# Performance work log

Hardware: AMD Instinct MI355X
Metric: run time of the kernel (lower is better)

The kernel has to match this reference:

```python
import jax, jax.numpy as jnp
import numpy as np

H, D = 8, 128           # num_heads, head_dim
HID = 1024              # hidden_size
K = 4                   # short conv kernel
EPS_QK = 1e-6
EPS_NORM = 1e-5


def short_conv(x, w):
    # x: (B, T, C), w: (C, 1, K) depthwise causal conv (zero initial state) + SiLU
    k = w.shape[-1]
    xp = jnp.pad(x, ((0, 0), (k - 1, 0), (0, 0)))
    xc = jnp.transpose(xp, (0, 2, 1))  # (B, C, T+K-1)
    y = jax.lax.conv_general_dilated(xc, w, window_strides=(1,), padding='VALID',
                                     feature_group_count=w.shape[0])
    return jax.nn.silu(jnp.transpose(y, (0, 2, 1)))


def _rmsn(t, eps):
    return t * jax.lax.rsqrt(jnp.mean(t * t, axis=-1, keepdims=True) + eps)


def setup_inputs() -> dict:
    key = jax.random.key(0)
    ks = jax.random.split(key, 16)
    s = 0.02
    inp = {
        'x': jax.random.normal(ks[0], (2, 1024, HID), dtype=jnp.float32),
        'Wq': jax.random.normal(ks[1], (H * D, HID), dtype=jnp.float32) * s,
        'Wk': jax.random.normal(ks[2], (H * D, HID), dtype=jnp.float32) * s,
        'Wv': jax.random.normal(ks[3], (H * D, HID), dtype=jnp.float32) * s,
        'wq_conv': jax.random.normal(ks[4], (H * D, 1, K), dtype=jnp.float32) * 0.3,
        'wk_conv': jax.random.normal(ks[5], (H * D, 1, K), dtype=jnp.float32) * 0.3,
        'wv_conv': jax.random.normal(ks[6], (H * D, 1, K), dtype=jnp.float32) * 0.3,
        'Wfa': jax.random.normal(ks[7], (D, HID), dtype=jnp.float32) * s,
        'Wfb': jax.random.normal(ks[8], (H * D, D), dtype=jnp.float32) * s,
        'Wb': jax.random.normal(ks[9], (H, HID), dtype=jnp.float32) * s,
        'Wga': jax.random.normal(ks[10], (D, HID), dtype=jnp.float32) * s,
        'Wgb': jax.random.normal(ks[11], (H * D, D), dtype=jnp.float32) * s,
        'A_log': jnp.log(jax.random.uniform(ks[12], (H,), minval=1.0, maxval=16.0, dtype=jnp.float32)),
        'dt_bias': jnp.zeros((H, D), dtype=jnp.float32),
        'o_norm_w': jnp.ones((D,), dtype=jnp.float32),
        'Wo': jax.random.normal(ks[13], (HID, H * D), dtype=jnp.float32) * s,
    }
    return inp


def reference(x, Wq, Wk, Wv, wq_conv, wk_conv, wv_conv, Wfa, Wfb, Wb, Wga, Wgb,
              A_log, dt_bias, o_norm_w, Wo):
    B, T, _ = x.shape
    scale = float(D) ** -0.5

    q = short_conv(x @ Wq.T, wq_conv).reshape(B, T, H, D)
    k = short_conv(x @ Wk.T, wk_conv).reshape(B, T, H, D)
    v = short_conv(x @ Wv.T, wv_conv).reshape(B, T, H, D)

    q = (scale ** 2) * _rmsn(q, EPS_QK)
    k = scale * _rmsn(k, EPS_QK)

    a_logits = ((x @ Wfa.T) @ Wfb.T).reshape(B, T, H, D)
    g = -jnp.exp(A_log)[None, None, :, None] * jax.nn.softplus(a_logits + dt_bias)  # (B,T,H,D)
    beta = jax.nn.sigmoid(x @ Wb.T)  # (B,T,H)

    # gated delta-rule recurrence over time; state S: (B, H, Dk, Dv)
    def step(S, inputs):
        q_t, k_t, v_t, g_t, b_t = inputs
        S = S * jnp.exp(g_t)[..., None]                       # per-channel decay on key dim
        kv = jnp.einsum('bhd,bhdv->bhv', k_t, S)              # read
        delta = b_t[..., None] * (v_t - kv)                   # beta-gated delta
        S = S + k_t[..., None] * delta[:, :, None, :]         # rank-1 write
        o = jnp.einsum('bhd,bhdv->bhv', q_t, S)
        return S, o

    tb = lambda t: jnp.moveaxis(t, 1, 0)  # (B,T,...) -> (T,B,...)
    S0 = jnp.zeros((B, H, D, D), dtype=x.dtype)
    _, o_t = jax.lax.scan(step, S0, (tb(q), tb(k), tb(v), tb(g), tb(beta)))
    out = jnp.moveaxis(o_t, 0, 1)  # (B, T, H, D)

    gate = ((x @ Wga.T) @ Wgb.T).reshape(B, T, H, D)
    out = _rmsn(out, EPS_NORM) * o_norm_w * jax.nn.sigmoid(gate)
    return out.reshape(B, T, H * D) @ Wo.T
```

## Files before the change

### kernel.cpp

```cpp
#include <hip/hip_runtime.h>
#include <hip/hip_bf16.h>
#include <math.h>

#define H 8
#define D 128
#define HID 1024
#define KCONV 4
#define G 8

typedef __bf16 bhalf;
typedef __bf16 bhalf4 __attribute__((ext_vector_type(4)));
typedef __bf16 bhalf8 __attribute__((ext_vector_type(8)));
typedef float f32x4 __attribute__((ext_vector_type(4)));
typedef float f32x2 __attribute__((ext_vector_type(2)));

__device__ __forceinline__ void async16(const void* g, void* l) {
    __builtin_amdgcn_global_load_lds(
        (const __attribute__((address_space(1))) void*)g,
        (__attribute__((address_space(3))) void*)l, 16, 0, 0);
}
__device__ __forceinline__ void async4(const void* g, void* l) {
    __builtin_amdgcn_global_load_lds(
        (const __attribute__((address_space(1))) void*)g,
        (__attribute__((address_space(3))) void*)l, 4, 0, 0);
}

__device__ __forceinline__ f32x4 ds2_b64(const float* p) {
    f32x4 r;
    asm volatile("ds_read2_b64 %0, %1 offset0:0 offset1:64"
                 : "=v"(r)
                 : "v"((const __attribute__((address_space(3))) float*)p));
    return r;
}
__device__ __forceinline__ f32x2 ds2_b32_o128(const float* p) {
    f32x2 r;
    asm volatile("ds_read2_b32 %0, %1 offset0:0 offset1:128"
                 : "=v"(r)
                 : "v"((const __attribute__((address_space(3))) float*)p));
    return r;
}
__device__ __forceinline__ f32x2 ds2_b32_o1(const float* p) {
    f32x2 r;
    asm volatile("ds_read2_b32 %0, %1 offset0:0 offset1:1"
                 : "=v"(r)
                 : "v"((const __attribute__((address_space(3))) float*)p));
    return r;
}

__global__ __launch_bounds__(256) void gemm_bf16_nt(const bhalf* A, const bhalf* B,
                                                    void* Cv,
                                                    int M, int N, int K,
                                                    int lda, int ldb, int ldc, int epi,
                                                    const float* __restrict__ A_log,
                                                    const float* __restrict__ dt_bias,
                                                    const bhalf* A2, const bhalf* B2,
                                                    void* C2, int epi2,
                                                    bhalf* __restrict__ pXAG,
                                                    float* __restrict__ pBETA)
{
    if (blockIdx.z) { A = A2; B = B2; Cv = C2; epi = epi2; }
    __shared__ __align__(16) bhalf As[128][32];
    __shared__ __align__(16) bhalf Bs[64][32];
    int tid = threadIdx.x;
    int wid = tid >> 6, lane = tid & 63;
    int rowBase = blockIdx.y * 128;
    int colBase = blockIdx.x * 64;
    int wm = wid >> 1, wn = wid & 1;

    f32x4 acc[4][2] = {};

    int r = lane >> 2;
    int cseg = lane & 3;

    for (int k0 = 0; k0 < K; k0 += 32) {
        __syncthreads();
#pragma unroll
        for (int s = 0; s < 3; ++s) {
            int j = wid * 3 + s;
            if (j < 8) {
                const bhalf* ga = A + (size_t)(rowBase + j * 16 + r) * lda + k0 + cseg * 8;
                async16(ga, &As[j * 16][0]);
            } else {
                int jb = j - 8;
                const bhalf* ga = B + (size_t)(colBase + jb * 16 + r) * ldb + k0 + cseg * 8;
                async16(ga, &Bs[jb * 16][0]);
            }
        }
        __syncthreads();
        int mq = lane & 15, kq = (lane >> 4) * 8;
        bhalf8 af[4], bfr[2];
#pragma unroll
        for (int mt = 0; mt < 4; ++mt)
            af[mt] = *(const bhalf8*)&As[wm * 64 + mt * 16 + mq][kq];
#pragma unroll
        for (int nt = 0; nt < 2; ++nt)
            bfr[nt] = *(const bhalf8*)&Bs[wn * 32 + nt * 16 + mq][kq];
#pragma unroll
        for (int mt = 0; mt < 4; ++mt)
#pragma unroll
            for (int nt = 0; nt < 2; ++nt)
                acc[mt][nt] = __builtin_amdgcn_mfma_f32_16x16x32_bf16(
                    af[mt], bfr[nt], acc[mt][nt], 0, 0, 0);
    }
    int rquad = (lane >> 4) * 4;
#pragma unroll
    for (int mt = 0; mt < 4; ++mt) {
        int m0 = rowBase + wm * 64 + mt * 16 + rquad;
#pragma unroll
        for (int nt = 0; nt < 2; ++nt) {
            int c = colBase + wn * 32 + (lane & 15) + nt * 16;
#pragma unroll
            for (int rr = 0; rr < 4; ++rr) {
                float val = acc[mt][nt][rr];
                int m = m0 + rr;
                if (epi == 0) {
                    ((float*)Cv)[(size_t)m * ldc + c] = val;
                } else if (epi == 1) {
                    int h = c >> 7, d = c & 127;
                    float z = val + dt_bias[h * D + d];
                    float sp = (z > 20.f) ? z : log1pf(expf(z));
                    ((float*)Cv)[(size_t)m * ldc + c] = expf(-expf(A_log[h]) * sp);
                } else if (epi == 2) {
                    ((bhalf*)Cv)[(size_t)m * ldc + c] = (bhalf)val;
                } else {
                    if (c < 3072) {
                        ((float*)Cv)[(size_t)m * 3072 + c] = val;
                    } else if (c < 3328) {
                        pXAG[(size_t)m * 256 + (c - 3072)] = (bhalf)val;
                    } else if (c < 3336) {
                        pBETA[(size_t)m * 8 + (c - 3328)] = 1.f / (1.f + expf(-val));
                    }
                }
            }
        }
    }
}

__global__ void cast1(const float* __restrict__ s, bhalf* __restrict__ d, int n4)
{
    int i = blockIdx.x * blockDim.x + threadIdx.x;
    if (i >= n4) return;
    float4 v = ((const float4*)s)[i];
    bhalf4 o = {(bhalf)v.x, (bhalf)v.y, (bhalf)v.z, (bhalf)v.w};
    ((bhalf4*)d)[i] = o;
}
__global__ void cast4(const float* __restrict__ s0, const float* __restrict__ s1,
                      const float* __restrict__ s2, const float* __restrict__ s3,
                      bhalf* __restrict__ d0, bhalf* __restrict__ d1,
                      bhalf* __restrict__ d2, bhalf* __restrict__ d3, int n4)
{
    int i = blockIdx.x * blockDim.x + threadIdx.x;
    if (i >= n4) return;
    int a = blockIdx.y;
    const float* s = (a == 0) ? s0 : (a == 1) ? s1 : (a == 2) ? s2 : s3;
    bhalf* d = (a == 0) ? d0 : (a == 1) ? d1 : (a == 2) ? d2 : d3;
    float4 v = ((const float4*)s)[i];
    bhalf4 o = {(bhalf)v.x, (bhalf)v.y, (bhalf)v.z, (bhalf)v.w};
    ((bhalf4*)d)[i] = o;
}

__global__ __launch_bounds__(128) void conv3_kernel(const float* __restrict__ QKV,
                                                    const float* __restrict__ wq,
                                                    const float* __restrict__ wk,
                                                    const float* __restrict__ wv,
                                                    float* __restrict__ Qc,
                                                    float* __restrict__ Kc,
                                                    float* __restrict__ Vc,
                                                    int T)
{
    int which = blockIdx.y;
    const float* w; float* out; int mode; float scale;
    if (which == 0)      { w = wq; out = Qc; mode = 1; scale = 1.0f / 128.0f; }
    else if (which == 1) { w = wk; out = Kc; mode = 1; scale = 0.08838834764831845f; }
    else                 { w = wv; out = Vc; mode = 0; scale = 1.f; }

    int bid = blockIdx.x;
    int h = bid % H;
    int t = (bid / H) % T;
    int b = bid / (H * T);
    int d = threadIdx.x;
    int c = h * D + d;
    const float* base = QKV + (size_t)b * T * 3072 + which * 1024 + c;
    float acc = 0.f;
#pragma unroll
    for (int j = 0; j < KCONV; ++j) {
        int tt = t - (KCONV - 1) + j;
        float xv = (tt >= 0) ? base[(size_t)tt * 3072] : 0.f;
        acc += xv * w[c * KCONV + j];
    }
    float y = acc / (1.f + expf(-acc));
    if (mode) {
        __shared__ float red[2];
        float ss = y * y;
#pragma unroll
        for (int s = 32; s > 0; s >>= 1) ss += __shfl_xor(ss, s, 64);
        if ((threadIdx.x & 63) == 0) red[threadIdx.x >> 6] = ss;
        __syncthreads();
        float tot = red[0] + red[1];
        float r = rsqrtf(tot * (1.f / D) + 1e-6f);
        y = y * r * scale;
    }
    out[(size_t)bid * D + d] = y;
}

template <int CTRL>
__device__ __forceinline__ float dpp_add(float x) {
    int y = __builtin_amdgcn_update_dpp(0, __builtin_bit_cast(int, x),
                                        CTRL, 0xF, 0xF, false);
    return x + __builtin_bit_cast(float, y);
}
__device__ __forceinline__ float wave_sum63(float x) {
    x = dpp_add<0x111>(x);
    x = dpp_add<0x112>(x);
    x = dpp_add<0x114>(x);
    x = dpp_add<0x118>(x);
    x = dpp_add<0x142>(x);
    x = dpp_add<0x143>(x);
    return x;
}
__device__ __forceinline__ float wave_sum(float x) {
    return __builtin_bit_cast(float,
        __builtin_amdgcn_readlane(__builtin_bit_cast(int, wave_sum63(x)), 63));
}

__global__ __launch_bounds__(256, 2) void recur_cols_kernel(const float* __restrict__ Q,
                                                            const float* __restrict__ Kc,
                                                            const float* __restrict__ V,
                                                            const float* __restrict__ EG,
                                                            const float* __restrict__ BETA,
                                                            float* __restrict__ O,
                                                            int T)
{
    __shared__ __align__(16) float lds[2][4][G][128];
    __shared__ __align__(16) float ldsb[2][64];

    int wid = threadIdx.x >> 6;
    int lane = threadIdx.x & 63;
    int gw = blockIdx.x * 4 + wid;
    int bh = gw >> 7;
    int col = gw & 127;
    int b = bh >> 3, h = bh & 7;

    size_t base = ((size_t)b * T * H + h) * D;
    const char* slab0;
    if (wid == 0)      slab0 = (const char*)(Kc + base);
    else if (wid == 1) slab0 = (const char*)(Q + base);
    else if (wid == 2) slab0 = (const char*)(EG + base);
    else               slab0 = (const char*)(V + base);
    const char* betaPtr = (const char*)(BETA + (size_t)b * T * H + h);
    float* Ob = O + base + col;

    int d0 = lane * 2;
    float S0 = 0.f, S1 = 0.f;
    const int strideT = H * D;
    int rsel = lane >> 5;
    int seg = (lane & 31) * 16;
    int ngroups = T / G;

#pragma unroll
    for (int j = 0; j < 4; ++j) {
        int t = j * 2 + rsel;
        async16(slab0 + (size_t)t * 4096 + seg, &lds[0][wid][j * 2][0]);
    }
    if (wid == 3) {
        int t = lane & 7;
        async4(betaPtr + (size_t)t * (H * 4), &ldsb[0][0]);
    }

    for (int g = 0; g < ngroups; ++g) {
        int bf = g & 1;
        __syncthreads();
        if (g + 1 < ngroups) {
            int t0 = (g + 1) * G;
#pragma unroll
            for (int j = 0; j < 4; ++j) {
                int t = t0 + j * 2 + rsel;
                async16(slab0 + (size_t)t * 4096 + seg, &lds[bf ^ 1][wid][j * 2][0]);
            }
            if (wid == 3) {
                int t = t0 + (lane & 7);
                async4(betaPtr + (size_t)t * (H * 4), &ldsb[bf ^ 1][0]);
            }
        }
        f32x4 K4[4], E4[4], Q4[4];
        f32x2 V2[4], B2[4];
#pragma unroll
        for (int p = 0; p < 4; ++p) K4[p] = ds2_b64(&lds[bf][0][2 * p][d0]);
#pragma unroll
        for (int p = 0; p < 4; ++p) E4[p] = ds2_b64(&lds[bf][2][2 * p][d0]);
#pragma unroll
        for (int p = 0; p < 4; ++p) V2[p] = ds2_b32_o128(&lds[bf][3][2 * p][col]);
#pragma unroll
        for (int p = 0; p < 4; ++p) B2[p] = ds2_b32_o1(&ldsb[bf][2 * p]);
#pragma unroll
        for (int p = 0; p < 4; ++p) Q4[p] = ds2_b64(&lds[bf][1][2 * p][d0]);

        asm volatile("s_waitcnt lgkmcnt(12)"
            : "+v"(K4[0]), "+v"(K4[1]), "+v"(K4[2]), "+v"(K4[3]),
              "+v"(E4[0]), "+v"(E4[1]), "+v"(E4[2]), "+v"(E4[3]));
        asm volatile("s_waitcnt lgkmcnt(4)"
            : "+v"(V2[0]), "+v"(V2[1]), "+v"(V2[2]), "+v"(V2[3]),
              "+v"(B2[0]), "+v"(B2[1]), "+v"(B2[2]), "+v"(B2[3]));
        asm volatile("s_waitcnt lgkmcnt(0)"
            : "+v"(Q4[0]), "+v"(Q4[1]), "+v"(Q4[2]), "+v"(Q4[3]));

        float kx[G], ky[G], ex[G], ey[G], qx[G], qy[G], vg[G], bg[G];
#pragma unroll
        for (int p = 0; p < 4; ++p) {
            kx[2 * p] = K4[p].x; ky[2 * p] = K4[p].y;
            kx[2 * p + 1] = K4[p].z; ky[2 * p + 1] = K4[p].w;
            ex[2 * p] = E4[p].x; ey[2 * p] = E4[p].y;
            ex[2 * p + 1] = E4[p].z; ey[2 * p + 1] = E4[p].w;
            qx[2 * p] = Q4[p].x; qy[2 * p] = Q4[p].y;
            qx[2 * p + 1] = Q4[p].z; qy[2 * p + 1] = Q4[p].w;
            vg[2 * p] = V2[p].x; vg[2 * p + 1] = V2[p].y;
            bg[2 * p] = B2[p].x; bg[2 * p + 1] = B2[p].y;
        }
        float kbx[G], kby[G], bv[G];
#pragma unroll
        for (int i = 0; i < G; ++i) {
            kbx[i] = kx[i] * ex[i] * bg[i];
            kby[i] = ky[i] * ey[i] * bg[i];
            bv[i]  = bg[i] * vg[i];
        }
        float og[G];
#pragma unroll
        for (int i = 0; i < G; ++i) {
            float R1 = wave_sum(kbx[i] * S0 + kby[i] * S1);
            float delta = bv[i] - R1;
            S0 = fmaf(ex[i], S0, kx[i] * delta);
            S1 = fmaf(ey[i], S1, ky[i] * delta);
            og[i] = wave_sum63(qx[i] * S0 + qy[i] * S1);
        }
        if (lane == 63) {
#pragma unroll
            for (int i = 0; i < G; ++i)
                Ob[(size_t)(g * G + i) * strideT] = og[i];
        }
    }
}

__global__ __launch_bounds__(128) void outnorm_kernel(const float* __restrict__ O,
                                                      const float* __restrict__ GATE,
                                                      const float* __restrict__ w,
                                                      bhalf* __restrict__ Obf)
{
    int bid = blockIdx.x;
    int d = threadIdx.x;
    size_t base = (size_t)bid * D;
    float y = O[base + d];
    __shared__ float red[2];
    float ss = y * y;
#pragma unroll
    for (int s = 32; s > 0; s >>= 1) ss += __shfl_xor(ss, s, 64);
    if ((threadIdx.x & 63) == 0) red[threadIdx.x >> 6] = ss;
    __syncthreads();
    float tot = red[0] + red[1];
    float r = rsqrtf(tot * (1.f / D) + 1e-5f);
    float gz = GATE[base + d];
    float sg = 1.f / (1.f + expf(-gz));
    Obf[base + d] = (bhalf)(y * r * w[d] * sg);
}

extern "C" void kernel_launch(void* const* d_in, const int* in_sizes, int n_in,
                              void* d_out, int out_size, void* d_ws, size_t ws_size,
                              hipStream_t stream)
{
    const float* x       = (const float*)d_in[0];
    const float* Wq      = (const float*)d_in[1];
    const float* Wk      = (const float*)d_in[2];
    const float* Wv      = (const float*)d_in[3];
    const float* wq_conv = (const float*)d_in[4];
    const float* wk_conv = (const float*)d_in[5];
    const float* wv_conv = (const float*)d_in[6];
    const float* Wfa     = (const float*)d_in[7];
    const float* Wfb     = (const float*)d_in[8];
    const float* Wb      = (const float*)d_in[9];
    const float* Wga     = (const float*)d_in[10];
    const float* Wgb     = (const float*)d_in[11];
    const float* A_log   = (const float*)d_in[12];
    const float* dt_bias = (const float*)d_in[13];
    const float* o_norm_w= (const float*)d_in[14];
    const float* Wo      = (const float*)d_in[15];

    int BT = in_sizes[0] / HID;
    int T = 1024;
    int B_ = BT / T;
    size_t M = (size_t)BT;
    size_t sz_big = M * HID;
    const int nW = HID * HID;
    const int nS = D * HID;
    const int NCAT = 3392;

    float* fp = (float*)d_ws;
    float* QKVp = fp;               fp += 3 * sz_big;
    float* Qc   = fp;               fp += sz_big;
    float* Kc   = fp;               fp += sz_big;
    float* Vc   = fp;               fp += sz_big;
    float* EGb  = fp;               fp += sz_big;
    float* GATE = fp;               fp += sz_big;
    float* Obuf = fp;               fp += sz_big;
    float* BETA = fp;               fp += M * H;
    bhalf* bp = (bhalf*)fp;
    bhalf* xb   = bp;               bp += sz_big;
    bhalf* Wcat = bp;               bp += (size_t)NCAT * HID;
    bhalf* Wob  = bp;               bp += nW;
    bhalf* Wfbb = bp;               bp += nS;
    bhalf* Wgbb = bp;               bp += nS;
    bhalf* XAG  = bp;               bp += M * 256;
    bhalf* Obf  = bp;               bp += sz_big;

    dim3 blk(256);

    cast1<<<(int)((sz_big / 4 + 255) / 256), 256, 0, stream>>>(x, xb, (int)(sz_big / 4));
    cast4<<<dim3((nW / 4 + 255) / 256, 4), 256, 0, stream>>>(Wq, Wk, Wv, Wo,
        Wcat, Wcat + nW, Wcat + 2 * (size_t)nW, Wob, nW / 4);
    cast4<<<dim3((nS / 4 + 255) / 256, 4), 256, 0, stream>>>(Wfa, Wga, Wfb, Wgb,
        Wcat + 3 * (size_t)nW, Wcat + 3 * (size_t)nW + nS, Wfbb, Wgbb, nS / 4);
    cast1<<<(H * HID / 4 + 255) / 256, 256, 0, stream>>>(Wb,
        Wcat + 3 * (size_t)nW + 2 * (size_t)nS, H * HID / 4);

    gemm_bf16_nt<<<dim3(NCAT / 64, BT / 128), blk, 0, stream>>>(
        xb, Wcat, QKVp, BT, NCAT, HID, HID, HID, 3072, 3, nullptr, nullptr,
        nullptr, nullptr, nullptr, 0, XAG, BETA);

    conv3_kernel<<<dim3(BT * H, 3), 128, 0, stream>>>(QKVp,
                                                      wq_conv, wk_conv, wv_conv,
                                                      Qc, Kc, Vc, T);

    gemm_bf16_nt<<<dim3(HID / 64, BT / 128, 2), blk, 0, stream>>>(
        XAG, Wfbb, EGb, BT, HID, D, 256, D, HID, 1, A_log, dt_bias,
        XAG + D, Wgbb, GATE, 0, nullptr, nullptr);

    recur_cols_kernel<<<B_ * H * 32, 256, 0, stream>>>(Qc, Kc, Vc, EGb, BETA, Obuf, T);

    outnorm_kernel<<<BT * H, 128, 0, stream>>>(Obuf, GATE, o_norm_w, Obf);

    gemm_bf16_nt<<<dim3(HID / 64, BT / 128), blk, 0, stream>>>(
        Obf, Wob, (float*)d_out, BT, HID, HID, HID, HID, HID, 0, nullptr, nullptr,
        nullptr, nullptr, nullptr, 0, nullptr, nullptr);
}
```

Before: 381.6 us.

## Replace sequential delta-rule recurrence with chunked WY form and MFMA scan

Result: faster. 331.2 us (-13.2%).

```diff
diff --git a/kernel.cpp b/kernel.cpp
--- a/kernel.cpp
+++ b/kernel.cpp
@@ -6,45 +6,19 @@
 #define D 128
 #define HID 1024
 #define KCONV 4
-#define G 8
 
 typedef __bf16 bhalf;
 typedef __bf16 bhalf4 __attribute__((ext_vector_type(4)));
 typedef __bf16 bhalf8 __attribute__((ext_vector_type(8)));
 typedef float f32x4 __attribute__((ext_vector_type(4)));
-typedef float f32x2 __attribute__((ext_vector_type(2)));
+typedef _Float16 hlf;
+typedef _Float16 half8 __attribute__((ext_vector_type(8)));
+typedef _Float16 half4v __attribute__((ext_vector_type(4)));
 
 __device__ __forceinline__ void async16(const void* g, void* l) {
     __builtin_amdgcn_global_load_lds(
         (const __attribute__((address_space(1))) void*)g,
         (__attribute__((address_space(3))) void*)l, 16, 0, 0);
-}
-__device__ __forceinline__ void async4(const void* g, void* l) {
-    __builtin_amdgcn_global_load_lds(
-        (const __attribute__((address_space(1))) void*)g,
-        (__attribute__((address_space(3))) void*)l, 4, 0, 0);
-}
-
-__device__ __forceinline__ f32x4 ds2_b64(const float* p) {
-    f32x4 r;
-    asm volatile("ds_read2_b64 %0, %1 offset0:0 offset1:64"
-                 : "=v"(r)
-                 : "v"((const __attribute__((address_space(3))) float*)p));
-    return r;
-}
-__device__ __forceinline__ f32x2 ds2_b32_o128(const float* p) {
-    f32x2 r;
-    asm volatile("ds_read2_b32 %0, %1 offset0:0 offset1:128"
-                 : "=v"(r)
-                 : "v"((const __attribute__((address_space(3))) float*)p));
-    return r;
-}
-__device__ __forceinline__ f32x2 ds2_b32_o1(const float* p) {
-    f32x2 r;
-    asm volatile("ds_read2_b32 %0, %1 offset0:0 offset1:1"
-                 : "=v"(r)
-                 : "v"((const __attribute__((address_space(3))) float*)p));
-    return r;
 }
 
 __global__ __launch_bounds__(256) void gemm_bf16_nt(const bhalf* A, const bhalf* B,
@@ -218,125 +192,219 @@
     x = dpp_add<0x143>(x);
     return x;
 }
-__device__ __forceinline__ float wave_sum(float x) {
-    return __builtin_bit_cast(float,
-        __builtin_amdgcn_readlane(__builtin_bit_cast(int, wave_sum63(x)), 63));
-}
-
-__global__ __launch_bounds__(256, 2) void recur_cols_kernel(const float* __restrict__ Q,
-                                                            const float* __restrict__ Kc,
-                                                            const float* __restrict__ V,
-                                                            const float* __restrict__ EG,
-                                                            const float* __restrict__ BETA,
-                                                            float* __restrict__ O,
-                                                            int T)
-{
-    __shared__ __align__(16) float lds[2][4][G][128];
-    __shared__ __align__(16) float ldsb[2][64];
-
-    int wid = threadIdx.x >> 6;
-    int lane = threadIdx.x & 63;
-    int gw = blockIdx.x * 4 + wid;
-    int bh = gw >> 7;
-    int col = gw & 127;
+
+
+__global__ __launch_bounds__(256) void chunk_prep_kernel(
+    const float* __restrict__ Q, const float* __restrict__ K,
+    const float* __restrict__ V, const float* __restrict__ E,
+    const float* __restrict__ BETA,
+    hlf* __restrict__ Wn, float* __restrict__ Uf, hlf* __restrict__ Qt,
+    hlf* __restrict__ AoL, hlf* __restrict__ KbT, float* __restrict__ Aend,
+    int T)
+{
+    __shared__ __align__(16) float e_s[32][128];
+    __shared__ __align__(16) float k_s[32][128];
+    __shared__ __align__(16) float U_s[32][128];
+    __shared__ __align__(16) hlf  A_s[32][128];
+    __shared__ __align__(16) hlf  W_s[32][128];
+    __shared__ float P_s[32][32];
+    __shared__ float Ao_s[32][32];
+    __shared__ float beta_s[32];
+
+    int tid = threadIdx.x, wid = tid >> 6, lane = tid & 63;
+    int bid = blockIdx.x;
+    int bh = bid >> 5, ch = bid & 31;
     int b = bh >> 3, h = bh & 7;
-
-    size_t base = ((size_t)b * T * H + h) * D;
-    const char* slab0;
-    if (wid == 0)      slab0 = (const char*)(Kc + base);
-    else if (wid == 1) slab0 = (const char*)(Q + base);
-    else if (wid == 2) slab0 = (const char*)(EG + base);
-    else               slab0 = (const char*)(V + base);
-    const char* betaPtr = (const char*)(BETA + (size_t)b * T * H + h);
-    float* Ob = O + base + col;
-
+    int t0 = ch * 32;
+    size_t rowb = (size_t)(b * T + t0) * 1024 + h * 128;
+    size_t co = (size_t)bh * 32 + ch;
+
+    int rs2 = lane >> 5, seg = (lane & 31) * 4;
+#pragma unroll
+    for (int p = wid * 4; p < wid * 4 + 4; ++p) {
+        int row = p * 2 + rs2;
+        async16(E + rowb + (size_t)row * 1024 + seg, &e_s[p * 2][0]);
+        async16(K + rowb + (size_t)row * 1024 + seg, &k_s[p * 2][0]);
+    }
+    __syncthreads();
+
+    for (int x = tid; x < 1024; x += 256) Ao_s[x >> 5][x & 31] = 0.f;
+    if (wid == 2 && lane < 32)
+        beta_s[lane] = BETA[(size_t)(b * T + t0 + lane) * 8 + h];
     int d0 = lane * 2;
-    float S0 = 0.f, S1 = 0.f;
-    const int strideT = H * D;
-    int rsel = lane >> 5;
-    int seg = (lane & 31) * 16;
-    int ngroups = T / G;
-
-#pragma unroll
-    for (int j = 0; j < 4; ++j) {
-        int t = j * 2 + rsel;
-        async16(slab0 + (size_t)t * 4096 + seg, &lds[0][wid][j * 2][0]);
-    }
-    if (wid == 3) {
-        int t = lane & 7;
-        async4(betaPtr + (size_t)t * (H * 4), &ldsb[0][0]);
-    }
-
-    for (int g = 0; g < ngroups; ++g) {
-        int bf = g & 1;
+    if (wid == 0) {
+        float a0 = 1.f, a1 = 1.f;
+        for (int t = 0; t < 32; ++t) {
+            a0 *= e_s[t][d0]; a1 *= e_s[t][d0 + 1];
+            A_s[t][d0] = (hlf)a0; A_s[t][d0 + 1] = (hlf)a1;
+        }
+        Aend[co * 128 + d0] = a0; Aend[co * 128 + d0 + 1] = a1;
+    } else if (wid == 1) {
+        float s0 = 1.f, s1 = 1.f;
+        for (int t = 31; t >= 0; --t) {
+            KbT[co * 4096 + (size_t)d0 * 32 + t]       = (hlf)(k_s[t][d0] * s0);
+            KbT[co * 4096 + (size_t)(d0 + 1) * 32 + t] = (hlf)(k_s[t][d0 + 1] * s1);
+            s0 *= e_s[t][d0]; s1 *= e_s[t][d0 + 1];
+        }
+    }
+    __syncthreads();
+
+#pragma unroll
+    for (int ii = 0; ii < 8; ++ii) {
+        int i = wid + ii * 4;
+        float ki0 = k_s[i][d0], ki1 = k_s[i][d0 + 1];
+        float2 qv = *(const float2*)(Q + rowb + (size_t)i * 1024 + d0);
+        float aa = wave_sum63(qv.x * ki0 + qv.y * ki1);
+        if (lane == 63) Ao_s[i][i] = aa;
+        float R0 = 1.f, R1 = 1.f;
+        for (int j = i - 1; j >= 0; --j) {
+            R0 *= e_s[j + 1][d0]; R1 *= e_s[j + 1][d0 + 1];
+            float u0 = R0 * k_s[j][d0], u1 = R1 * k_s[j][d0 + 1];
+            float pp = wave_sum63(ki0 * u0 + ki1 * u1);
+            float a2 = wave_sum63(qv.x * u0 + qv.y * u1);
+            if (lane == 63) { P_s[i][j] = pp; Ao_s[i][j] = a2; }
+        }
+    }
+    __syncthreads();
+
+    for (int x = tid; x < 1024; x += 256) {
+        int i2 = x >> 5, j2 = x & 31;
+        P_s[i2][j2] = (j2 < i2) ? P_s[i2][j2] * beta_s[i2] : 0.f;
+    }
+    __syncthreads();
+
+    if (wid == 0) {
+        for (int i = 0; i < 32; ++i) {
+            float bb = beta_s[i];
+            float a0 = bb * k_s[i][d0] * (float)A_s[i][d0];
+            float a1 = bb * k_s[i][d0 + 1] * (float)A_s[i][d0 + 1];
+            for (int k2 = 0; k2 < i; ++k2) {
+                float L = P_s[i][k2];
+                a0 -= L * (float)W_s[k2][d0];
+                a1 -= L * (float)W_s[k2][d0 + 1];
+            }
+            W_s[i][d0] = (hlf)a0; W_s[i][d0 + 1] = (hlf)a1;
+        }
+    } else if (wid == 1) {
+        for (int i = 0; i < 32; ++i) {
+            float bb = beta_s[i];
+            float2 vv = *(const float2*)(V + rowb + (size_t)i * 1024 + d0);
+            float a0 = bb * vv.x, a1 = bb * vv.y;
+            for (int k2 = 0; k2 < i; ++k2) {
+                float L = P_s[i][k2];
+                a0 -= L * U_s[k2][d0];
+                a1 -= L * U_s[k2][d0 + 1];
+            }
+            U_s[i][d0] = a0; U_s[i][d0 + 1] = a1;
+        }
+    } else {
+        for (int r2 = wid - 2; r2 < 32; r2 += 2) {
+            float2 qv = *(const float2*)(Q + rowb + (size_t)r2 * 1024 + d0);
+            Qt[co * 4096 + (size_t)r2 * 128 + d0]     = (hlf)(qv.x * (float)A_s[r2][d0]);
+            Qt[co * 4096 + (size_t)r2 * 128 + d0 + 1] = (hlf)(qv.y * (float)A_s[r2][d0 + 1]);
+        }
+    }
+    __syncthreads();
+
+    for (int x = tid; x < 4096; x += 256) {
+        Wn[co * 4096 + x] = (hlf)(-(float)W_s[x >> 7][x & 127]);
+        Uf[co * 4096 + x] = U_s[x >> 7][x & 127];
+    }
+    for (int x = tid; x < 1024; x += 256)
+        AoL[co * 1024 + x] = (hlf)Ao_s[x >> 5][x & 31];
+}
+
+__global__ __launch_bounds__(256) void chunk_scan_kernel(
+    const hlf* __restrict__ Wn, const float* __restrict__ Uf,
+    const hlf* __restrict__ Qt, const hlf* __restrict__ Ao,
+    const hlf* __restrict__ KbT, const float* __restrict__ Aend,
+    float* __restrict__ O, int T)
+{
+    __shared__ __align__(16) float Sf[32][132];
+    __shared__ __align__(16) hlf  Sh[32][136];
+    __shared__ __align__(16) hlf  Dt[32][40];
+    __shared__ float Ae[128];
+
+    int tid = threadIdx.x, wid = tid >> 6, lane = tid & 63;
+    int nbh = gridDim.x >> 2;
+    int bh = blockIdx.x % nbh, vs = blockIdx.x / nbh;
+    int b = bh >> 3, h = bh & 7;
+    int v0 = vs * 32;
+
+    for (int r = wid; r < 32; r += 4) {
+        for (int c2 = lane; c2 < 132; c2 += 64) Sf[r][c2] = 0.f;
+        for (int c2 = lane; c2 < 136; c2 += 64) Sh[r][c2] = (hlf)0.f;
+    }
+    __syncthreads();
+
+    int mq = lane & 15, kq = (lane >> 4) * 8, rq = (lane >> 4) * 4;
+    int tr = (wid >> 1) * 16, vc = (wid & 1) * 16;
+    int vr2 = (wid >> 1) * 16, dh2 = (wid & 1) * 64;
+
+    for (int c = 0; c < 32; ++c) {
+        size_t co = (size_t)bh * 32 + c;
+        const hlf*   Wc  = Wn  + co * 4096;
+        const float* Uc  = Uf  + co * 4096;
+        const hlf*   Qc2 = Qt  + co * 4096;
+        const hlf*   Aoc = Ao  + co * 1024;
+        const hlf*   Kbc = KbT + co * 4096;
+        if (tid < 128) Ae[tid] = Aend[co * 128 + tid];
+
+        f32x4 dacc;
+#pragma unroll
+        for (int rr = 0; rr < 4; ++rr)
+            dacc[rr] = Uc[(size_t)(tr + rq + rr) * 128 + v0 + vc + mq];
+#pragma unroll
+        for (int ks = 0; ks < 4; ++ks) {
+            half8 aw = *(const half8*)&Wc[(size_t)(tr + mq) * 128 + ks * 32 + kq];
+            half8 bs = *(const half8*)&Sh[vc + mq][ks * 32 + kq];
+            dacc = __builtin_amdgcn_mfma_f32_16x16x32_f16(aw, bs, dacc, 0, 0, 0);
+        }
+        half4v dh4;
+#pragma unroll
+        for (int rr = 0; rr < 4; ++rr) dh4[rr] = (hlf)dacc[rr];
+        *(half4v*)&Dt[vc + mq][tr + rq] = dh4;
         __syncthreads();
-        if (g + 1 < ngroups) {
-            int t0 = (g + 1) * G;
-#pragma unroll
-            for (int j = 0; j < 4; ++j) {
-                int t = t0 + j * 2 + rsel;
-                async16(slab0 + (size_t)t * 4096 + seg, &lds[bf ^ 1][wid][j * 2][0]);
+
+        f32x4 oacc = {0.f, 0.f, 0.f, 0.f};
+#pragma unroll
+        for (int ks = 0; ks < 4; ++ks) {
+            half8 aq = *(const half8*)&Qc2[(size_t)(tr + mq) * 128 + ks * 32 + kq];
+            half8 bs = *(const half8*)&Sh[vc + mq][ks * 32 + kq];
+            oacc = __builtin_amdgcn_mfma_f32_16x16x32_f16(aq, bs, oacc, 0, 0, 0);
+        }
+        {
+            half8 aA = *(const half8*)&Aoc[(tr + mq) * 32 + kq];
+            half8 bD = *(const half8*)&Dt[vc + mq][kq];
+            oacc = __builtin_amdgcn_mfma_f32_16x16x32_f16(aA, bD, oacc, 0, 0, 0);
+        }
+#pragma unroll
+        for (int rr = 0; rr < 4; ++rr)
+            O[((size_t)(b * T + c * 32 + tr + rq + rr) * 8 + h) * 128 + v0 + vc + mq]
+                = oacc[rr];
+
+        f32x4 sacc[4];
+        half8 aD = *(const half8*)&Dt[vr2 + mq][kq];
+#pragma unroll
+        for (int nt = 0; nt < 4; ++nt) {
+            int dc = dh2 + nt * 16 + mq;
+#pragma unroll
+            for (int rr = 0; rr < 4; ++rr)
+                sacc[nt][rr] = Sf[vr2 + rq + rr][dc] * Ae[dc];
+            half8 bK = *(const half8*)&Kbc[(size_t)dc * 32 + kq];
+            sacc[nt] = __builtin_amdgcn_mfma_f32_16x16x32_f16(aD, bK, sacc[nt], 0, 0, 0);
+        }
+        __syncthreads();
+#pragma unroll
+        for (int nt = 0; nt < 4; ++nt) {
+            int dc = dh2 + nt * 16 + mq;
+#pragma unroll
+            for (int rr = 0; rr < 4; ++rr) {
+                Sf[vr2 + rq + rr][dc] = sacc[nt][rr];
+                Sh[vr2 + rq + rr][dc] = (hlf)sacc[nt][rr];
             }
-            if (wid == 3) {
-                int t = t0 + (lane & 7);
-                async4(betaPtr + (size_t)t * (H * 4), &ldsb[bf ^ 1][0]);
-            }
-        }
-        f32x4 K4[4], E4[4], Q4[4];
-        f32x2 V2[4], B2[4];
-#pragma unroll
-        for (int p = 0; p < 4; ++p) K4[p] = ds2_b64(&lds[bf][0][2 * p][d0]);
-#pragma unroll
-        for (int p = 0; p < 4; ++p) E4[p] = ds2_b64(&lds[bf][2][2 * p][d0]);
-#pragma unroll
-        for (int p = 0; p < 4; ++p) V2[p] = ds2_b32_o128(&lds[bf][3][2 * p][col]);
-#pragma unroll
-        for (int p = 0; p < 4; ++p) B2[p] = ds2_b32_o1(&ldsb[bf][2 * p]);
-#pragma unroll
-        for (int p = 0; p < 4; ++p) Q4[p] = ds2_b64(&lds[bf][1][2 * p][d0]);
-
-        asm volatile("s_waitcnt lgkmcnt(12)"
-            : "+v"(K4[0]), "+v"(K4[1]), "+v"(K4[2]), "+v"(K4[3]),
-              "+v"(E4[0]), "+v"(E4[1]), "+v"(E4[2]), "+v"(E4[3]));
-        asm volatile("s_waitcnt lgkmcnt(4)"
-            : "+v"(V2[0]), "+v"(V2[1]), "+v"(V2[2]), "+v"(V2[3]),
-              "+v"(B2[0]), "+v"(B2[1]), "+v"(B2[2]), "+v"(B2[3]));
-        asm volatile("s_waitcnt lgkmcnt(0)"
-            : "+v"(Q4[0]), "+v"(Q4[1]), "+v"(Q4[2]), "+v"(Q4[3]));
-
-        float kx[G], ky[G], ex[G], ey[G], qx[G], qy[G], vg[G], bg[G];
-#pragma unroll
-        for (int p = 0; p < 4; ++p) {
-            kx[2 * p] = K4[p].x; ky[2 * p] = K4[p].y;
-            kx[2 * p + 1] = K4[p].z; ky[2 * p + 1] = K4[p].w;
-            ex[2 * p] = E4[p].x; ey[2 * p] = E4[p].y;
-            ex[2 * p + 1] = E4[p].z; ey[2 * p + 1] = E4[p].w;
-            qx[2 * p] = Q4[p].x; qy[2 * p] = Q4[p].y;
-            qx[2 * p + 1] = Q4[p].z; qy[2 * p + 1] = Q4[p].w;
-            vg[2 * p] = V2[p].x; vg[2 * p + 1] = V2[p].y;
-            bg[2 * p] = B2[p].x; bg[2 * p + 1] = B2[p].y;
-        }
-        float kbx[G], kby[G], bv[G];
-#pragma unroll
-        for (int i = 0; i < G; ++i) {
-            kbx[i] = kx[i] * ex[i] * bg[i];
-            kby[i] = ky[i] * ey[i] * bg[i];
-            bv[i]  = bg[i] * vg[i];
-        }
-        float og[G];
-#pragma unroll
-        for (int i = 0; i < G; ++i) {
-            float R1 = wave_sum(kbx[i] * S0 + kby[i] * S1);
-            float delta = bv[i] - R1;
-            S0 = fmaf(ex[i], S0, kx[i] * delta);
-            S1 = fmaf(ey[i], S1, ky[i] * delta);
-            og[i] = wave_sum63(qx[i] * S0 + qy[i] * S1);
-        }
-        if (lane == 63) {
-#pragma unroll
-            for (int i = 0; i < G; ++i)
-                Ob[(size_t)(g * G + i) * strideT] = og[i];
-        }
+        }
+        __syncthreads();
     }
 }
 
@@ -432,7 +500,18 @@
         XAG, Wfbb, EGb, BT, HID, D, 256, D, HID, 1, A_log, dt_bias,
         XAG + D, Wgbb, GATE, 0, nullptr, nullptr);
 
-    recur_cols_kernel<<<B_ * H * 32, 256, 0, stream>>>(Qc, Kc, Vc, EGb, BETA, Obuf, T);
+    int nbh = B_ * 8;
+    float* Uf   = QKVp;
+    float* Aend = Uf + (size_t)nbh * 32 * 4096;
+    hlf* Wn  = (hlf*)(Aend + (size_t)nbh * 32 * 128);
+    hlf* Qt  = Wn  + (size_t)nbh * 32 * 4096;
+    hlf* AoLp= Qt  + (size_t)nbh * 32 * 4096;
+    hlf* KbT = AoLp + (size_t)nbh * 32 * 1024;
+
+    chunk_prep_kernel<<<nbh * 32, 256, 0, stream>>>(Qc, Kc, Vc, EGb, BETA,
+                                                    Wn, Uf, Qt, AoLp, KbT, Aend, T);
+    chunk_scan_kernel<<<nbh * 4, 256, 0, stream>>>(Wn, Uf, Qt, AoLp, KbT, Aend,
+                                                   Obuf, T);
 
     outnorm_kernel<<<BT * H, 128, 0, stream>>>(Obuf, GATE, o_norm_w, Obf);
 
```
